# Performance work log

Measured on AMD Instinct MI355X. Metric: run time of the kernel, lower is better.

The kernel has to match this reference:

```python
import jax, jax.numpy as jnp
import numpy as np

N = 50000
E = 1600000
IN_C = 512
HID = 64
OUT_C = 64
HEADS = 2
K = 2
NEG_SLOPE = 0.2


def setup_inputs() -> dict:
    key = jax.random.key(0)
    ks = jax.random.split(key, 9)
    x = jax.random.normal(ks[0], (N, IN_C), dtype=jnp.float32)
    edge_index = jax.random.randint(ks[1], (2, E), 0, N, dtype=jnp.int64)
    edge_attr = jax.random.uniform(ks[2], (E,), dtype=jnp.float32)
    # SGConv linear (glorot-ish init)
    W_sg = jax.random.normal(ks[3], (IN_C, HID), dtype=jnp.float32) / np.sqrt(IN_C)
    b_sg = jnp.zeros((HID,), dtype=jnp.float32)
    # GATConv: lin (no bias), attention vectors, output bias (concat=False -> size OUT_C)
    W_gat = jax.random.normal(ks[4], (HID, HEADS * OUT_C), dtype=jnp.float32) / np.sqrt(HID)
    att_src = jax.random.normal(ks[5], (HEADS, OUT_C), dtype=jnp.float32) / np.sqrt(OUT_C)
    att_dst = jax.random.normal(ks[6], (HEADS, OUT_C), dtype=jnp.float32) / np.sqrt(OUT_C)
    b_gat = jnp.zeros((OUT_C,), dtype=jnp.float32)
    return {"x": x, "edge_index": edge_index, "edge_attr": edge_attr,
            "W_sg": W_sg, "b_sg": b_sg, "W_gat": W_gat,
            "att_src": att_src, "att_dst": att_dst, "b_gat": b_gat}


def reference(x, edge_index, edge_attr, W_sg, b_sg, W_gat, att_src, att_dst, b_gat):
    n = x.shape[0]
    src, dst = edge_index[0], edge_index[1]
    # add self-loops (weight 1) once; reused by SGConv (gcn_norm) and GAT
    loop = jnp.arange(n, dtype=src.dtype)
    src2 = jnp.concatenate([src, loop])
    dst2 = jnp.concatenate([dst, loop])
    ew = jnp.concatenate([edge_attr, jnp.ones((n,), x.dtype)])

    # ---- SGConv: K hops of D^-1/2 A D^-1/2, then linear ----
    deg = jax.ops.segment_sum(ew, dst2, num_segments=n)
    dinv = jnp.where(deg > 0, jax.lax.rsqrt(deg), 0.0)
    norm = dinv[src2] * ew * dinv[dst2]  # [E+N]
    h = x
    for _ in range(K):
        h = jax.ops.segment_sum(norm[:, None] * h[src2], dst2, num_segments=n)
    h = h @ W_sg + b_sg  # [N, HID]

    # activation (SELU); dropout is identity in eval mode
    h = jax.nn.selu(h)

    # ---- GATConv (heads, concat=False -> mean over heads) ----
    g = (h @ W_gat).reshape(n, HEADS, OUT_C)  # [N, H, C]
    a_src = jnp.einsum('nhc,hc->nh', g, att_src)  # [N, H]
    a_dst = jnp.einsum('nhc,hc->nh', g, att_dst)
    e = jax.nn.leaky_relu(a_src[src2] + a_dst[dst2], NEG_SLOPE)  # [E+N, H]
    # per-destination softmax (numerically stable)
    emax = jax.ops.segment_max(e, dst2, num_segments=n)
    emax = jnp.where(jnp.isfinite(emax), emax, 0.0)
    ee = jnp.exp(e - emax[dst2])
    denom = jax.ops.segment_sum(ee, dst2, num_segments=n)
    alpha = ee / jnp.maximum(denom[dst2], 1e-16)  # [E+N, H]
    out = jax.ops.segment_sum(alpha[:, :, None] * g[src2], dst2, num_segments=n)  # [N, H, C]
    return out.mean(axis=1) + b_gat  # [N, OUT_C]
```

## Files before the change

kernel.cpp:

```cpp
#include <hip/hip_runtime.h>
#include <hip/hip_fp16.h>
#include <math.h>

#define N_NODES 50000
#define N_EDGES 1600000
#define IN_CH 512
#define HID 64
#define OUTC 64
#define NEG_SLOPE 0.2f
#define EA_SCALE 131072.0f
#define PCAP 128
#define NBUCK 196
#define NB1 782
#define NSCAN (NBUCK * NB1)

typedef __attribute__((ext_vector_type(8))) short bf16x8;
typedef __attribute__((ext_vector_type(4))) float f32x4;

__device__ __forceinline__ unsigned bf16r(float f) {
    unsigned b = __float_as_uint(f);
    return (b + 0x7FFFu + ((b >> 16) & 1u)) >> 16;
}

__device__ __forceinline__ void gload16(const void* g, void* l) {
    __builtin_amdgcn_global_load_lds(
        (const __attribute__((address_space(1))) void*)g,
        (__attribute__((address_space(3))) void*)l, 16, 0, 0);
}

__device__ __forceinline__ float2 h2f2(unsigned u) {
    return __half22float2(*(__half2*)&u);
}

__global__ void k_wsplit(const float* __restrict__ W, short* __restrict__ Wfrag) {
    int idx = blockIdx.x * 256 + threadIdx.x;
    if (idx >= IN_CH * HID) return;
    int k = idx >> 6, c = idx & 63;
    float wv = W[idx];
    unsigned h = bf16r(wv);
    float res = wv - __uint_as_float(h << 16);
    unsigned l = bf16r(res);
    int kstep = k >> 5, cb = c >> 4;
    int lane = (c & 15) | (((k >> 3) & 3) << 4);
    int j = k & 7;
    int base = ((kstep * 4 + cb) * 2) * 512 + lane * 8 + j;
    Wfrag[base] = (short)h;
    Wfrag[base + 512] = (short)l;
}

#define G1R 64
#define G1KC 64
__global__ __launch_bounds__(256) void k_gemm_p1a(const float* __restrict__ x,
                                                  const short* __restrict__ Wfrag,
                                                  __half* __restrict__ p,
                                                  const int* __restrict__ dst,
                                                  int* __restrict__ gh) {
    __shared__ float xs[2][G1R][G1KC];
    __shared__ int hist[NBUCK];
    int tid = threadIdx.x;
    int bid = blockIdx.x;

    if (bid & 1) {
        int blk = bid >> 1;
        for (int j = tid; j < NBUCK; j += 256) hist[j] = 0;
        __syncthreads();
        int e0 = blk * 2048;
        int e1 = e0 + 2048; if (e1 > N_EDGES) e1 = N_EDGES;
        for (int e = e0 + tid; e < e1; e += 256)
            atomicAdd(&hist[((unsigned)dst[e]) >> 8], 1);
        __syncthreads();
        for (int j = tid; j < NBUCK; j += 256)
            gh[j * NB1 + blk] = hist[j];
        return;
    }

    int lane = tid & 63, wv = tid >> 6;
    int r0 = (bid >> 1) * G1R;
    f32x4 acc0 = {0.f, 0.f, 0.f, 0.f};
    f32x4 acc1 = {0.f, 0.f, 0.f, 0.f};
    f32x4 acc2 = {0.f, 0.f, 0.f, 0.f};
    f32x4 acc3 = {0.f, 0.f, 0.f, 0.f};

    auto stage = [&](int b, int k0) {
#pragma unroll
        for (int it = 0; it < 4; it++) {
            int rowbase = it * 16 + wv * 4;
            int row = rowbase + (lane >> 4);
            int gr = r0 + row; if (gr > N_NODES - 1) gr = N_NODES - 1;
            int col = ((lane & 15) ^ (row & 7)) << 2;
            gload16(x + (size_t)gr * IN_CH + k0 + col, &xs[b][rowbase][0]);
        }
    };

    auto loadB = [&](int ks, bf16x8& h0, bf16x8& l0, bf16x8& h1, bf16x8& l1,
                     bf16x8& h2, bf16x8& l2, bf16x8& h3, bf16x8& l3) {
        const short* wb = Wfrag + ks * 4096 + (lane << 3);
        h0 = *(const bf16x8*)(wb);        l0 = *(const bf16x8*)(wb + 512);
        h1 = *(const bf16x8*)(wb + 1024); l1 = *(const bf16x8*)(wb + 1536);
        h2 = *(const bf16x8*)(wb + 2048); l2 = *(const bf16x8*)(wb + 2560);
        h3 = *(const bf16x8*)(wb + 3072); l3 = *(const bf16x8*)(wb + 3584);
    };

    bf16x8 Xh0, Xl0, Xh1, Xl1, Xh2, Xl2, Xh3, Xl3;
    bf16x8 Yh0, Yl0, Yh1, Yl1, Yh2, Yl2, Yh3, Yl3;

    stage(0, 0);
    loadB(0, Xh0, Xl0, Xh1, Xl1, Xh2, Xl2, Xh3, Xl3);
    asm volatile("s_waitcnt vmcnt(0)" ::: "memory");
    __syncthreads();

    int cur = 0;
    int arow = wv * 16 + (lane & 15);
    const char* xsbase = (const char*)&xs[0][0][0];
    for (int k0 = 0; k0 < IN_CH; k0 += G1KC) {
        if (k0 + G1KC < IN_CH) stage(cur ^ 1, k0 + G1KC);
        int ks0 = k0 >> 5;

        loadB(ks0 + 1, Yh0, Yl0, Yh1, Yl1, Yh2, Yl2, Yh3, Yl3);
        {
            int c16 = ((lane >> 4) << 1);
            size_t rb = (size_t)cur * (G1R * G1KC * 4) + (size_t)arow * (G1KC * 4);
            float4 xa = *(const float4*)(xsbase + rb + (((c16    ) ^ (arow & 7)) << 4));
            float4 xb = *(const float4*)(xsbase + rb + (((c16 + 1) ^ (arow & 7)) << 4));
            float xv[8] = {xa.x, xa.y, xa.z, xa.w, xb.x, xb.y, xb.z, xb.w};
            bf16x8 ah, al;
#pragma unroll
            for (int j = 0; j < 8; j++) {
                unsigned b = __float_as_uint(xv[j]);
                float res = xv[j] - __uint_as_float(b & 0xFFFF0000u);
                ah[j] = (short)(b >> 16);
                al[j] = (short)(__float_as_uint(res) >> 16);
            }
            acc0 = __builtin_amdgcn_mfma_f32_16x16x32_bf16(ah, Xh0, acc0, 0, 0, 0);
            acc0 = __builtin_amdgcn_mfma_f32_16x16x32_bf16(ah, Xl0, acc0, 0, 0, 0);
            acc0 = __builtin_amdgcn_mfma_f32_16x16x32_bf16(al, Xh0, acc0, 0, 0, 0);
            acc1 = __builtin_amdgcn_mfma_f32_16x16x32_bf16(ah, Xh1, acc1, 0, 0, 0);
            acc1 = __builtin_amdgcn_mfma_f32_16x16x32_bf16(ah, Xl1, acc1, 0, 0, 0);
            acc1 = __builtin_amdgcn_mfma_f32_16x16x32_bf16(al, Xh1, acc1, 0, 0, 0);
            acc2 = __builtin_amdgcn_mfma_f32_16x16x32_bf16(ah, Xh2, acc2, 0, 0, 0);
            acc2 = __builtin_amdgcn_mfma_f32_16x16x32_bf16(ah, Xl2, acc2, 0, 0, 0);
            acc2 = __builtin_amdgcn_mfma_f32_16x16x32_bf16(al, Xh2, acc2, 0, 0, 0);
            acc3 = __builtin_amdgcn_mfma_f32_16x16x32_bf16(ah, Xh3, acc3, 0, 0, 0);
            acc3 = __builtin_amdgcn_mfma_f32_16x16x32_bf16(ah, Xl3, acc3, 0, 0, 0);
            acc3 = __builtin_amdgcn_mfma_f32_16x16x32_bf16(al, Xh3, acc3, 0, 0, 0);
        }

        if (k0 + G1KC < IN_CH)
            loadB(ks0 + 2, Xh0, Xl0, Xh1, Xl1, Xh2, Xl2, Xh3, Xl3);
        {
            int c16 = 8 + ((lane >> 4) << 1);
            size_t rb = (size_t)cur * (G1R * G1KC * 4) + (size_t)arow * (G1KC * 4);
            float4 xa = *(const float4*)(xsbase + rb + (((c16    ) ^ (arow & 7)) << 4));
            float4 xb = *(const float4*)(xsbase + rb + (((c16 + 1) ^ (arow & 7)) << 4));
            float xv[8] = {xa.x, xa.y, xa.z, xa.w, xb.x, xb.y, xb.z, xb.w};
            bf16x8 ah, al;
#pragma unroll
            for (int j = 0; j < 8; j++) {
                unsigned b = __float_as_uint(xv[j]);
                float res = xv[j] - __uint_as_float(b & 0xFFFF0000u);
                ah[j] = (short)(b >> 16);
                al[j] = (short)(__float_as_uint(res) >> 16);
            }
            acc0 = __builtin_amdgcn_mfma_f32_16x16x32_bf16(ah, Yh0, acc0, 0, 0, 0);
            acc0 = __builtin_amdgcn_mfma_f32_16x16x32_bf16(ah, Yl0, acc0, 0, 0, 0);
            acc0 = __builtin_amdgcn_mfma_f32_16x16x32_bf16(al, Yh0, acc0, 0, 0, 0);
            acc1 = __builtin_amdgcn_mfma_f32_16x16x32_bf16(ah, Yh1, acc1, 0, 0, 0);
            acc1 = __builtin_amdgcn_mfma_f32_16x16x32_bf16(ah, Yl1, acc1, 0, 0, 0);
            acc1 = __builtin_amdgcn_mfma_f32_16x16x32_bf16(al, Yh1, acc1, 0, 0, 0);
            acc2 = __builtin_amdgcn_mfma_f32_16x16x32_bf16(ah, Yh2, acc2, 0, 0, 0);
            acc2 = __builtin_amdgcn_mfma_f32_16x16x32_bf16(ah, Yl2, acc2, 0, 0, 0);
            acc2 = __builtin_amdgcn_mfma_f32_16x16x32_bf16(al, Yh2, acc2, 0, 0, 0);
            acc3 = __builtin_amdgcn_mfma_f32_16x16x32_bf16(ah, Yh3, acc3, 0, 0, 0);
            acc3 = __builtin_amdgcn_mfma_f32_16x16x32_bf16(ah, Yl3, acc3, 0, 0, 0);
            acc3 = __builtin_amdgcn_mfma_f32_16x16x32_bf16(al, Yh3, acc3, 0, 0, 0);
        }
        asm volatile("s_waitcnt vmcnt(0)" ::: "memory");
        __syncthreads();
        cur ^= 1;
    }
    int crow = r0 + wv * 16 + ((lane >> 4) << 2);
    int ccol = lane & 15;
#pragma unroll
    for (int r = 0; r < 4; r++) {
        int gr = crow + r;
        if (gr < N_NODES) {
            p[(unsigned)gr * HID + ccol]      = __float2half(acc0[r]);
            p[(unsigned)gr * HID + 16 + ccol] = __float2half(acc1[r]);
            p[(unsigned)gr * HID + 32 + ccol] = __float2half(acc2[r]);
            p[(unsigned)gr * HID + 48 + ccol] = __float2half(acc3[r]);
        }
    }
}

__global__ void k_scan_reduce(const int* __restrict__ counts, int* bsum, int n) {
    __shared__ int lds[256];
    int i = blockIdx.x * 256 + threadIdx.x;
    lds[threadIdx.x] = (i < n) ? counts[i] : 0;
    __syncthreads();
    for (int s = 128; s > 0; s >>= 1) {
        if (threadIdx.x < s) lds[threadIdx.x] += lds[threadIdx.x + s];
        __syncthreads();
    }
    if (threadIdx.x == 0) bsum[blockIdx.x] = lds[0];
}

__global__ void k_scan_mid(int* bsum, int nb) {
    __shared__ int lds[256];
    __shared__ int carry;
    int t = threadIdx.x;
    if (t == 0) carry = 0;
    __syncthreads();
    for (int base = 0; base < nb; base += 256) {
        int i = base + t;
        int v = (i < nb) ? bsum[i] : 0;
        int orig = v;
        lds[t] = v;
        __syncthreads();
        for (int s = 1; s < 256; s <<= 1) {
            int add = (t >= s) ? lds[t - s] : 0;
            __syncthreads();
            lds[t] += add;
            __syncthreads();
        }
        int c = carry;
        if (i < nb) bsum[i] = lds[t] - orig + c;
        __syncthreads();
        if (t == 0) carry = c + lds[255];
        __syncthreads();
    }
}

__global__ void k_scan_final(const int* __restrict__ counts, const int* __restrict__ bsum,
                             int* __restrict__ outx, int n) {
    __shared__ int lds[256];
    int t = threadIdx.x;
    int i = blockIdx.x * 256 + t;
    int v = (i < n) ? counts[i] : 0;
    lds[t] = v;
    __syncthreads();
    for (int s = 1; s < 256; s <<= 1) {
        int add = (t >= s) ? lds[t - s] : 0;
        __syncthreads();
        lds[t] += add;
        __syncthreads();
    }
    if (i < n) outx[i] = bsum[blockIdx.x] + lds[t] - v;
}

__global__ __launch_bounds__(256) void k_p1b(const int* __restrict__ src,
                                             const int* __restrict__ dst,
                                             const float* __restrict__ ea,
                                             const int* __restrict__ ghs,
                                             int2* __restrict__ part) {
    __shared__ int curb[NBUCK];
    int tid = threadIdx.x;
    int blk = blockIdx.x;
    for (int j = tid; j < NBUCK; j += 256) curb[j] = ghs[j * NB1 + blk];
    __syncthreads();
    int e0 = blk * 2048;
    int e1 = e0 + 2048; if (e1 > N_EDGES) e1 = N_EDGES;
    for (int e = e0 + tid; e < e1; e += 256) {
        int s = src[e], d = dst[e];
        unsigned eb = __float_as_uint(ea[e]);
        int b = ((unsigned)d) >> 8;
        int pos = atomicAdd(&curb[b], 1);
        part[pos] = make_int2((s << 16) | (int)(eb & 0xFFFFu),
                              d | (int)(eb & 0xFFFF0000u));
    }
}

__global__ __launch_bounds__(256) void k_p2(const int2* __restrict__ part,
                                            const int* __restrict__ ghs,
                                            int* __restrict__ offs,
                                            float* __restrict__ dinv,
                                            int* __restrict__ edges4) {
    __shared__ int cnt[256];
    __shared__ unsigned degs[256];
    __shared__ int sc[256];
    int tid = threadIdx.x;
    int b = blockIdx.x;
    int vb = b << 8;
    int bs = ghs[b * NB1];
    int be = (b == NBUCK - 1) ? N_EDGES : ghs[(b + 1) * NB1];
    cnt[tid] = 0; degs[tid] = 0u;
    __syncthreads();
    for (int i = bs + tid; i < be; i += 256) {
        int2 r = part[i];
        int idx = r.y & 255;
        unsigned eb = ((unsigned)r.y & 0xFFFF0000u) | ((unsigned)r.x & 0xFFFFu);
        atomicAdd(&cnt[idx], 1);
        atomicAdd(&degs[idx], (unsigned)(__uint_as_float(eb) * EA_SCALE));
    }
    __syncthreads();
    sc[tid] = cnt[tid];
    __syncthreads();
    for (int s = 1; s < 256; s <<= 1) {
        int add = (tid >= s) ? sc[tid - s] : 0;
        __syncthreads();
        sc[tid] += add;
        __syncthreads();
    }
    int excl = sc[tid] - cnt[tid];
    int v = vb + tid;
    if (v < N_NODES) {
        offs[v] = bs + excl;
        dinv[v] = rsqrtf(1.0f + (float)degs[tid] * (1.0f / EA_SCALE));
    }
    cnt[tid] = bs + excl;
    __syncthreads();
    for (int i = bs + tid; i < be; i += 256) {
        int2 r = part[i];
        int idx = r.y & 255;
        unsigned eb = ((unsigned)r.y & 0xFFFF0000u) | ((unsigned)r.x & 0xFFFFu);
        int pos = atomicAdd(&cnt[idx], 1);
        int srec = (int)((unsigned)r.x >> 16);
        edges4[pos] = (srec << 16) |
                      (int)__half_as_ushort(__float2half_rn(__uint_as_float(eb)));
    }
    if (b == 0 && tid == 0) offs[N_NODES] = N_EDGES;
}

__global__ void k_hscale(unsigned* __restrict__ h2, const float* __restrict__ dinv) {
    int idx = blockIdx.x * 256 + threadIdx.x;
    if (idx >= N_NODES * 32) return;
    float dv = dinv[idx >> 5];
    unsigned u = h2[idx];
    float2 f = h2f2(u);
    __half2 r = __floats2half2_rn(f.x * dv, f.y * dv);
    h2[idx] = *(unsigned*)&r;
}

__global__ __launch_bounds__(256) void k_hop(const uint2* __restrict__ hin4,
                                             const int* __restrict__ offs,
                                             const int* __restrict__ edges4,
                                             const float* __restrict__ dinv,
                                             uint2* __restrict__ hout4,
                                             int pw) {
    __shared__ float4 part[2][16];
    int tid = threadIdx.x;
    int w = tid >> 6, lane = tid & 63;
    int slot = w >> 1, half = w & 1;
    int cl = lane & 15, es = lane >> 4;
    int v = blockIdx.x * 2 + slot;
    int beg = offs[v], end = offs[v + 1];
    int cnt = end - beg;
    int mid = beg + (cnt >> 1);
    int lo = half ? mid : beg;
    int hi = half ? end : mid;
    float a0 = 0.f, a1 = 0.f, a2 = 0.f, a3 = 0.f;
    float b0 = 0.f, b1 = 0.f, b2 = 0.f, b3 = 0.f;
    if (!half && !es) {
        uint2 u = hin4[(unsigned)v * 16 + cl];
        float2 f0 = h2f2(u.x), f1 = h2f2(u.y);
        a0 = f0.x; a1 = f0.y; a2 = f1.x; a3 = f1.y;
    }
    int i = lo;
    for (; i + 8 <= hi; i += 8) {
        int r0 = edges4[i + es];
        int r1 = edges4[i + 4 + es];
        uint2 g0 = hin4[(((unsigned)r0 >> 16) << 4) + cl];
        uint2 g1 = hin4[(((unsigned)r1 >> 16) << 4) + cl];
        float w0 = __half2float(__ushort_as_half((unsigned short)(r0 & 0xFFFF)));
        float w1 = __half2float(__ushort_as_half((unsigned short)(r1 & 0xFFFF)));
        float2 g0a = h2f2(g0.x), g0b = h2f2(g0.y);
        float2 g1a = h2f2(g1.x), g1b = h2f2(g1.y);
        a0 += w0 * g0a.x; a1 += w0 * g0a.y; a2 += w0 * g0b.x; a3 += w0 * g0b.y;
        b0 += w1 * g1a.x; b1 += w1 * g1a.y; b2 += w1 * g1b.x; b3 += w1 * g1b.y;
    }
    for (; i + es < hi; i += 4) {
        int r0 = edges4[i + es];
        uint2 g0 = hin4[(((unsigned)r0 >> 16) << 4) + cl];
        float w0 = __half2float(__ushort_as_half((unsigned short)(r0 & 0xFFFF)));
        float2 g0a = h2f2(g0.x), g0b = h2f2(g0.y);
        a0 += w0 * g0a.x; a1 += w0 * g0a.y; a2 += w0 * g0b.x; a3 += w0 * g0b.y;
    }
    a0 += b0; a1 += b1; a2 += b2; a3 += b3;
    a0 += __shfl_xor(a0, 16); a1 += __shfl_xor(a1, 16);
    a2 += __shfl_xor(a2, 16); a3 += __shfl_xor(a3, 16);
    a0 += __shfl_xor(a0, 32); a1 += __shfl_xor(a1, 32);
    a2 += __shfl_xor(a2, 32); a3 += __shfl_xor(a3, 32);
    if (half && lane < 16) part[slot][cl] = make_float4(a0, a1, a2, a3);
    __syncthreads();
    if (!half && lane < 16) {
        float dv = dinv[v];
        float sc = (pw == 2) ? dv * dv : dv;
        float4 pp = part[slot][cl];
        __half2 h0 = __floats2half2_rn(sc * (a0 + pp.x), sc * (a1 + pp.y));
        __half2 h1 = __floats2half2_rn(sc * (a2 + pp.z), sc * (a3 + pp.w));
        hout4[(unsigned)v * 16 + cl] = make_uint2(*(unsigned*)&h0, *(unsigned*)&h1);
    }
}

#define G2_ROWS 32
__global__ __launch_bounds__(256) void k_act_gemm2(const __half* __restrict__ h2,
                                                   const float* __restrict__ bsg,
                                                   const float* __restrict__ Wg,
                                                   const float* __restrict__ att_s,
                                                   const float* __restrict__ att_d,
                                                   uint2* __restrict__ g4h,
                                                   float2* __restrict__ asrc2,
                                                   float4* __restrict__ admm) {
    __shared__ float hs[G2_ROWS][HID];
    int tid = threadIdx.x;
    int wave = tid >> 6, lane = tid & 63;
    int r0 = blockIdx.x * G2_ROWS;
    int rbase = wave * 8;

    const float SC = 1.0507009873554805f, AL = 1.6732632423543772f;
    {
        int row = tid >> 3, c0 = (tid & 7) * 8;
        int r = r0 + row;
        float vals[8];
        if (r < N_NODES) {
            uint4 raw = *(const uint4*)(h2 + (unsigned)r * HID + c0);
            float2 f0 = h2f2(raw.x), f1 = h2f2(raw.y), f2 = h2f2(raw.z), f3 = h2f2(raw.w);
            vals[0] = f0.x; vals[1] = f0.y; vals[2] = f1.x; vals[3] = f1.y;
            vals[4] = f2.x; vals[5] = f2.y; vals[6] = f3.x; vals[7] = f3.y;
        } else {
#pragma unroll
            for (int j = 0; j < 8; j++) vals[j] = 0.f;
        }
#pragma unroll
        for (int j = 0; j < 8; j++) {
            float hv = vals[j] + bsg[c0 + j];
            hv = (hv > 0.f) ? SC * hv : SC * AL * (__expf(hv) - 1.f);
            hs[row][c0 + j] = hv;
        }
    }
    __syncthreads();

    float accx[8], accy[8];
#pragma unroll
    for (int j = 0; j < 8; j++) { accx[j] = 0.f; accy[j] = 0.f; }
#pragma unroll 2
    for (int k = 0; k < HID; k++) {
        float w0 = Wg[(size_t)k * 128 + lane];
        float w1 = Wg[(size_t)k * 128 + 64 + lane];
#pragma unroll
        for (int j = 0; j < 8; j++) {
            float hk = hs[rbase + j][k];
            accx[j] += hk * w0;
            accy[j] += hk * w1;
        }
    }
    float ats0 = att_s[lane], ats1 = att_s[64 + lane];
    float atd0 = att_d[lane], atd1 = att_d[64 + lane];
#pragma unroll
    for (int j = 0; j < 8; j++) {
        int v = r0 + rbase + j;
        if (v >= N_NODES) break;
        __half2 gp = __floats2half2_rn(accx[j], accy[j]);
        unsigned gpu = *(unsigned*)&gp;
        unsigned other = (unsigned)__shfl_xor((int)gpu, 1);
        if (!(lane & 1)) g4h[(unsigned)v * 32 + (lane >> 1)] = make_uint2(gpu, other);
        float s0 = accx[j] * ats0, s1 = accy[j] * ats1;
        float d0 = accx[j] * atd0, d1 = accy[j] * atd1;
#pragma unroll
        for (int o = 32; o > 0; o >>= 1) {
            s0 += __shfl_xor(s0, o);
            s1 += __shfl_xor(s1, o);
            d0 += __shfl_xor(d0, o);
            d1 += __shfl_xor(d1, o);
        }
        if (lane == 0) {
            asrc2[v] = make_float2(s0, s1);
            float m0 = s0 + d0; m0 = (m0 > 0.f) ? m0 : NEG_SLOPE * m0;
            float m1 = s1 + d1; m1 = (m1 > 0.f) ? m1 : NEG_SLOPE * m1;
            admm[v] = make_float4(d0, d1, m0, m1);
        }
    }
}

__global__ __launch_bounds__(256) void k_gat(const uint2* __restrict__ g4h,
                                             const float2* __restrict__ asrc2,
                                             const float4* __restrict__ admm,
                                             const int* __restrict__ offs,
                                             const int* __restrict__ edges4,
                                             const float* __restrict__ bgat,
                                             float* __restrict__ out) {
    __shared__ int4 pbuf[2][2][PCAP];
    __shared__ float4 pacc[2][32];
    __shared__ float2 pden[2][32];
    int tid = threadIdx.x;
    int w = tid >> 6, lane = tid & 63;
    int slot = w >> 1, half = w & 1;
    int cl = lane & 31, es = lane >> 5;
    int v = blockIdx.x * 2 + slot;
    float4 am = admm[v];
    int beg = offs[v], end = offs[v + 1];
    int cnt = end - beg;
    int mid = beg + (cnt >> 1);
    int lo = half ? mid : beg;
    int hi = half ? end : mid;
    int n = hi - lo;

    float pd0 = 0.f, pd1 = 0.f;
    for (int i = lo + lane; i < hi; i += 64) {
        int r = edges4[i];
        unsigned s = (unsigned)r >> 16;
        float2 a = asrc2[s];
        float t0 = a.x + am.x; t0 = (t0 > 0.f) ? t0 : NEG_SLOPE * t0;
        float t1 = a.y + am.y; t1 = (t1 > 0.f) ? t1 : NEG_SLOPE * t1;
        float p0 = __expf(t0 - am.z);
        float p1 = __expf(t1 - am.w);
        int idx = i - lo;
        if (idx < PCAP)
            pbuf[slot][half][idx] = make_int4((int)(s << 5), __float_as_int(p0), __float_as_int(p1), 0);
        pd0 += p0; pd1 += p1;
    }
#pragma unroll
    for (int o = 32; o > 0; o >>= 1) {
        pd0 += __shfl_xor(pd0, o);
        pd1 += __shfl_xor(pd1, o);
    }
    if (!half) { pd0 += 1.f; pd1 += 1.f; }

    float aA = 0.f, aB = 0.f, aC = 0.f, aD = 0.f;
    float bA = 0.f, bB = 0.f, bC = 0.f, bD = 0.f;
    if (!half && !es) {
        uint2 gs = g4h[(unsigned)v * 32 + cl];
        float2 gx = h2f2(gs.x), gy = h2f2(gs.y);
        aA = gx.x; aB = gx.y; aC = gy.x; aD = gy.y;
    }
    int n1 = (n < PCAP) ? n : PCAP;
    int ii = 0;
    for (; ii + 8 <= n1; ii += 8) {
        int4 e0 = pbuf[slot][half][ii + es];
        int4 e1 = pbuf[slot][half][ii + 2 + es];
        int4 e2 = pbuf[slot][half][ii + 4 + es];
        int4 e3 = pbuf[slot][half][ii + 6 + es];
        uint2 g0 = g4h[(unsigned)(e0.x + cl)];
        uint2 g1 = g4h[(unsigned)(e1.x + cl)];
        uint2 g2 = g4h[(unsigned)(e2.x + cl)];
        uint2 g3 = g4h[(unsigned)(e3.x + cl)];
        float p00 = __int_as_float(e0.y), p01 = __int_as_float(e0.z);
        float p10 = __int_as_float(e1.y), p11 = __int_as_float(e1.z);
        float p20 = __int_as_float(e2.y), p21 = __int_as_float(e2.z);
        float p30 = __int_as_float(e3.y), p31 = __int_as_float(e3.z);
        float2 g0x = h2f2(g0.x), g0y = h2f2(g0.y);
        float2 g1x = h2f2(g1.x), g1y = h2f2(g1.y);
        float2 g2x = h2f2(g2.x), g2y = h2f2(g2.y);
        float2 g3x = h2f2(g3.x), g3y = h2f2(g3.y);
        aA += p00 * g0x.x; aB += p01 * g0x.y; aC += p00 * g0y.x; aD += p01 * g0y.y;
        bA += p10 * g1x.x; bB += p11 * g1x.y; bC += p10 * g1y.x; bD += p11 * g1y.y;
        aA += p20 * g2x.x; aB += p21 * g2x.y; aC += p20 * g2y.x; aD += p21 * g2y.y;
        bA += p30 * g3x.x; bB += p31 * g3x.y; bC += p30 * g3y.x; bD += p31 * g3y.y;
    }
    for (; ii + es < n1; ii += 2) {
        int4 e0 = pbuf[slot][half][ii + es];
        uint2 g0 = g4h[(unsigned)(e0.x + cl)];
        float p00 = __int_as_float(e0.y), p01 = __int_as_float(e0.z);
        float2 g0x = h2f2(g0.x), g0y = h2f2(g0.y);
        aA += p00 * g0x.x; aB += p01 * g0x.y; aC += p00 * g0y.x; aD += p01 * g0y.y;
    }
    for (int jj = PCAP + es; jj < n; jj += 2) {
        int r = edges4[lo + jj];
        unsigned s = (unsigned)r >> 16;
        float2 a = asrc2[s];
        float t0 = a.x + am.x; t0 = (t0 > 0.f) ? t0 : NEG_SLOPE * t0;
        float t1 = a.y + am.y; t1 = (t1 > 0.f) ? t1 : NEG_SLOPE * t1;
        float p0 = __expf(t0 - am.z);
        float p1 = __expf(t1 - am.w);
        uint2 g0 = g4h[(s << 5) + cl];
        float2 g0x = h2f2(g0.x), g0y = h2f2(g0.y);
        aA += p0 * g0x.x; aB += p1 * g0x.y; aC += p0 * g0y.x; aD += p1 * g0y.y;
    }
    aA += bA; aB += bB; aC += bC; aD += bD;
    aA += __shfl_xor(aA, 32); aB += __shfl_xor(aB, 32);
    aC += __shfl_xor(aC, 32); aD += __shfl_xor(aD, 32);
    if (half && lane < 32) {
        pacc[slot][cl] = make_float4(aA, aB, aC, aD);
        pden[slot][cl] = make_float2(pd0, pd1);
    }
    __syncthreads();
    if (!half && lane < 32) {
        float4 pa = pacc[slot][cl];
        float2 pd = pden[slot][cl];
        float r0 = 1.f / (pd0 + pd.x), r1 = 1.f / (pd1 + pd.y);
        float oe = 0.5f * ((aA + pa.x) * r0 + (aB + pa.y) * r1) + bgat[cl * 2];
        float oo = 0.5f * ((aC + pa.z) * r0 + (aD + pa.w) * r1) + bgat[cl * 2 + 1];
        *(float2*)&out[(unsigned)v * OUTC + cl * 2] = make_float2(oe, oo);
    }
}

extern "C" void kernel_launch(void* const* d_in, const int* in_sizes, int n_in,
                              void* d_out, int out_size, void* d_ws, size_t ws_size,
                              hipStream_t stream) {
    const float* x     = (const float*)d_in[0];
    const int*   ei    = (const int*)d_in[1];
    const float* ea    = (const float*)d_in[2];
    const float* Wsg   = (const float*)d_in[3];
    const float* bsg   = (const float*)d_in[4];
    const float* Wg    = (const float*)d_in[5];
    const float* att_s = (const float*)d_in[6];
    const float* att_d = (const float*)d_in[7];
    const float* bgat  = (const float*)d_in[8];
    const int* src = ei;
    const int* dst = ei + N_EDGES;
    float* out = (float*)d_out;

    char* ws = (char*)d_ws;
    size_t off = 0;
    auto alloc = [&](size_t bytes) -> void* {
        void* p = ws + off;
        off = (off + bytes + 255) & ~(size_t)255;
        return p;
    };
    int*      gh     = (int*)alloc((size_t)NSCAN * 4);
    int*      ghs    = (int*)alloc((size_t)NSCAN * 4);
    int*      bsum   = (int*)alloc(1024 * 4);
    int2*     part   = (int2*)alloc((size_t)N_EDGES * 8);
    int*      edges4 = (int*)alloc((size_t)N_EDGES * 4);
    int*      offs   = (int*)alloc((size_t)(N_NODES + 1) * 4);
    float*    dinv   = (float*)alloc((size_t)N_NODES * 4);
    short*    Wfrag  = (short*)alloc((size_t)IN_CH * HID * 2 * 2);
    __half*   h0     = (__half*)alloc((size_t)N_NODES * HID * 2);
    __half*   h1     = (__half*)alloc((size_t)N_NODES * HID * 2);
    uint2*    g4h    = (uint2*)alloc((size_t)N_NODES * 32 * 8);
    float2*   asrc2  = (float2*)alloc((size_t)N_NODES * 8);
    float4*   admm   = (float4*)alloc((size_t)N_NODES * 16);
    (void)ws_size; (void)in_sizes; (void)n_in; (void)out_size;

    k_wsplit<<<(IN_CH * HID + 255) / 256, 256, 0, stream>>>(Wsg, Wfrag);

    k_gemm_p1a<<<2 * NB1, 256, 0, stream>>>(x, Wfrag, h0, dst, gh);

    int nb = (NSCAN + 255) / 256;
    k_scan_reduce<<<nb, 256, 0, stream>>>(gh, bsum, NSCAN);
    k_scan_mid<<<1, 256, 0, stream>>>(bsum, nb);
    k_scan_final<<<nb, 256, 0, stream>>>(gh, bsum, ghs, NSCAN);

    k_p1b<<<NB1, 256, 0, stream>>>(src, dst, ea, ghs, part);
    k_p2<<<NBUCK, 256, 0, stream>>>(part, ghs, offs, dinv, edges4);

    k_hscale<<<(N_NODES * 32 + 255) / 256, 256, 0, stream>>>((unsigned*)h0, dinv);

    k_hop<<<N_NODES / 2, 256, 0, stream>>>((const uint2*)h0, offs, edges4, dinv, (uint2*)h1, 2);
    k_hop<<<N_NODES / 2, 256, 0, stream>>>((const uint2*)h1, offs, edges4, dinv, (uint2*)h0, 1);
    k_act_gemm2<<<(N_NODES + G2_ROWS - 1) / G2_ROWS, 256, 0, stream>>>(h0, bsg, Wg, att_s, att_d, g4h, asrc2, admm);
    k_gat<<<N_NODES / 2, 256, 0, stream>>>(g4h, asrc2, admm, offs, edges4, bgat, out);
}
```

Before: 285.7 us.

## Shrink histogram grid, merge three-stage scan into one kernel, fuse hscale into p2

The edge histogram chunk grows from 2048 to 8192 edges, so the scan array drops from 782 to 196 columns per bucket. That makes a single 1024-thread block scan practical, replacing the reduce/mid/final three-kernel scan. The dinv scaling of h0 moves into k_p2, which already computes dinv per node, removing another launch. The intent is fewer launches and less scan work, at the cost of fewer histogram and partition blocks (k_p1b now runs only 196 blocks) and a serial single-block scan.

```diff
diff --git a/kernel.cpp b/kernel.cpp
--- a/kernel.cpp
+++ b/kernel.cpp
@@ -11,7 +11,8 @@
 #define EA_SCALE 131072.0f
 #define PCAP 128
 #define NBUCK 196
-#define NB1 782
+#define CHUNK 8192
+#define NB1 196
 #define NSCAN (NBUCK * NB1)
 
 typedef __attribute__((ext_vector_type(8))) short bf16x8;
@@ -62,10 +63,11 @@
 
     if (bid & 1) {
         int blk = bid >> 1;
+        if (blk >= NB1) return;
         for (int j = tid; j < NBUCK; j += 256) hist[j] = 0;
         __syncthreads();
-        int e0 = blk * 2048;
-        int e1 = e0 + 2048; if (e1 > N_EDGES) e1 = N_EDGES;
+        int e0 = blk * CHUNK;
+        int e1 = e0 + CHUNK; if (e1 > N_EDGES) e1 = N_EDGES;
         for (int e = e0 + tid; e < e1; e += 256)
             atomicAdd(&hist[((unsigned)dst[e]) >> 8], 1);
         __syncthreads();
@@ -192,59 +194,34 @@
     }
 }
 
-__global__ void k_scan_reduce(const int* __restrict__ counts, int* bsum, int n) {
-    __shared__ int lds[256];
-    int i = blockIdx.x * 256 + threadIdx.x;
-    lds[threadIdx.x] = (i < n) ? counts[i] : 0;
-    __syncthreads();
-    for (int s = 128; s > 0; s >>= 1) {
-        if (threadIdx.x < s) lds[threadIdx.x] += lds[threadIdx.x + s];
+__global__ __launch_bounds__(1024) void k_scan(const int* __restrict__ gh,
+                                               int* __restrict__ ghs) {
+    __shared__ int part[1024];
+    int t = threadIdx.x;
+    const int PER = (NSCAN + 1023) / 1024;
+    int base = t * PER;
+    int s = 0;
+    for (int i = 0; i < PER; i++) {
+        int idx = base + i;
+        if (idx < NSCAN) s += gh[idx];
+    }
+    part[t] = s;
+    __syncthreads();
+    for (int o = 1; o < 1024; o <<= 1) {
+        int add = (t >= o) ? part[t - o] : 0;
         __syncthreads();
-    }
-    if (threadIdx.x == 0) bsum[blockIdx.x] = lds[0];
-}
-
-__global__ void k_scan_mid(int* bsum, int nb) {
-    __shared__ int lds[256];
-    __shared__ int carry;
-    int t = threadIdx.x;
-    if (t == 0) carry = 0;
-    __syncthreads();
-    for (int base = 0; base < nb; base += 256) {
-        int i = base + t;
-        int v = (i < nb) ? bsum[i] : 0;
-        int orig = v;
-        lds[t] = v;
+        part[t] += add;
         __syncthreads();
-        for (int s = 1; s < 256; s <<= 1) {
-            int add = (t >= s) ? lds[t - s] : 0;
-            __syncthreads();
-            lds[t] += add;
-            __syncthreads();
-        }
-        int c = carry;
-        if (i < nb) bsum[i] = lds[t] - orig + c;
-        __syncthreads();
-        if (t == 0) carry = c + lds[255];
-        __syncthreads();
-    }
-}
-
-__global__ void k_scan_final(const int* __restrict__ counts, const int* __restrict__ bsum,
-                             int* __restrict__ outx, int n) {
-    __shared__ int lds[256];
-    int t = threadIdx.x;
-    int i = blockIdx.x * 256 + t;
-    int v = (i < n) ? counts[i] : 0;
-    lds[t] = v;
-    __syncthreads();
-    for (int s = 1; s < 256; s <<= 1) {
-        int add = (t >= s) ? lds[t - s] : 0;
-        __syncthreads();
-        lds[t] += add;
-        __syncthreads();
-    }
-    if (i < n) outx[i] = bsum[blockIdx.x] + lds[t] - v;
+    }
+    int run = part[t] - s;
+    for (int i = 0; i < PER; i++) {
+        int idx = base + i;
+        if (idx < NSCAN) {
+            int v = gh[idx];
+            ghs[idx] = run;
+            run += v;
+        }
+    }
 }
 
 __global__ __launch_bounds__(256) void k_p1b(const int* __restrict__ src,
@@ -257,8 +234,8 @@
     int blk = blockIdx.x;
     for (int j = tid; j < NBUCK; j += 256) curb[j] = ghs[j * NB1 + blk];
     __syncthreads();
-    int e0 = blk * 2048;
-    int e1 = e0 + 2048; if (e1 > N_EDGES) e1 = N_EDGES;
+    int e0 = blk * CHUNK;
+    int e1 = e0 + CHUNK; if (e1 > N_EDGES) e1 = N_EDGES;
     for (int e = e0 + tid; e < e1; e += 256) {
         int s = src[e], d = dst[e];
         unsigned eb = __float_as_uint(ea[e]);
@@ -273,10 +250,12 @@
                                             const int* __restrict__ ghs,
                                             int* __restrict__ offs,
                                             float* __restrict__ dinv,
-                                            int* __restrict__ edges4) {
+                                            int* __restrict__ edges4,
+                                            unsigned* __restrict__ h2) {
     __shared__ int cnt[256];
     __shared__ unsigned degs[256];
     __shared__ int sc[256];
+    __shared__ float dvs[256];
     int tid = threadIdx.x;
     int b = blockIdx.x;
     int vb = b << 8;
@@ -302,9 +281,11 @@
     }
     int excl = sc[tid] - cnt[tid];
     int v = vb + tid;
+    float dv = rsqrtf(1.0f + (float)degs[tid] * (1.0f / EA_SCALE));
+    dvs[tid] = dv;
     if (v < N_NODES) {
         offs[v] = bs + excl;
-        dinv[v] = rsqrtf(1.0f + (float)degs[tid] * (1.0f / EA_SCALE));
+        dinv[v] = dv;
     }
     cnt[tid] = bs + excl;
     __syncthreads();
@@ -317,17 +298,17 @@
         edges4[pos] = (srec << 16) |
                       (int)__half_as_ushort(__float2half_rn(__uint_as_float(eb)));
     }
+    int nn = N_NODES - vb; if (nn > 256) nn = 256; if (nn < 0) nn = 0;
+    int hcount = nn * 32;
+    unsigned hbase = (unsigned)vb * 32;
+    for (int i = tid; i < hcount; i += 256) {
+        float dvv = dvs[i >> 5];
+        unsigned u = h2[hbase + i];
+        float2 f = h2f2(u);
+        __half2 r = __floats2half2_rn(f.x * dvv, f.y * dvv);
+        h2[hbase + i] = *(unsigned*)&r;
+    }
     if (b == 0 && tid == 0) offs[N_NODES] = N_EDGES;
-}
-
-__global__ void k_hscale(unsigned* __restrict__ h2, const float* __restrict__ dinv) {
-    int idx = blockIdx.x * 256 + threadIdx.x;
-    if (idx >= N_NODES * 32) return;
-    float dv = dinv[idx >> 5];
-    unsigned u = h2[idx];
-    float2 f = h2f2(u);
-    __half2 r = __floats2half2_rn(f.x * dv, f.y * dv);
-    h2[idx] = *(unsigned*)&r;
 }
 
 __global__ __launch_bounds__(256) void k_hop(const uint2* __restrict__ hin4,
@@ -608,7 +589,6 @@
     };
     int*      gh     = (int*)alloc((size_t)NSCAN * 4);
     int*      ghs    = (int*)alloc((size_t)NSCAN * 4);
-    int*      bsum   = (int*)alloc(1024 * 4);
     int2*     part   = (int2*)alloc((size_t)N_EDGES * 8);
     int*      edges4 = (int*)alloc((size_t)N_EDGES * 4);
     int*      offs   = (int*)alloc((size_t)(N_NODES + 1) * 4);
@@ -623,17 +603,11 @@
 
     k_wsplit<<<(IN_CH * HID + 255) / 256, 256, 0, stream>>>(Wsg, Wfrag);
 
-    k_gemm_p1a<<<2 * NB1, 256, 0, stream>>>(x, Wfrag, h0, dst, gh);
-
-    int nb = (NSCAN + 255) / 256;
-    k_scan_reduce<<<nb, 256, 0, stream>>>(gh, bsum, NSCAN);
-    k_scan_mid<<<1, 256, 0, stream>>>(bsum, nb);
-    k_scan_final<<<nb, 256, 0, stream>>>(gh, bsum, ghs, NSCAN);
-
+    k_gemm_p1a<<<1564, 256, 0, stream>>>(x, Wfrag, h0, dst, gh);
+
+    k_scan<<<1, 1024, 0, stream>>>(gh, ghs);
     k_p1b<<<NB1, 256, 0, stream>>>(src, dst, ea, ghs, part);
-    k_p2<<<NBUCK, 256, 0, stream>>>(part, ghs, offs, dinv, edges4);
-
-    k_hscale<<<(N_NODES * 32 + 255) / 256, 256, 0, stream>>>((unsigned*)h0, dinv);
+    k_p2<<<NBUCK, 256, 0, stream>>>(part, ghs, offs, dinv, edges4, (unsigned*)h0);
 
     k_hop<<<N_NODES / 2, 256, 0, stream>>>((const uint2*)h0, offs, edges4, dinv, (uint2*)h1, 2);
     k_hop<<<N_NODES / 2, 256, 0, stream>>>((const uint2*)h1, offs, edges4, dinv, (uint2*)h0, 1);
```

After: 344.1 us. 1.2x slower.
